# Kernel optimization log

Measured on AMD Instinct MI355X. Metric: run time of the kernel, lower is better.

The kernel has to match this reference:

```python
import jax, jax.numpy as jnp
import numpy as np

Z_INDEX = 0.5  # from init_kwargs


def _masked_mean(v, z_index):
    # Torch: std_mean (unbiased std, ddof=1) over the whole vector, keep values
    # where (v - mean) > -z * std, then mean of kept values. Mask is no_grad.
    mean = jnp.mean(v, axis=-1, keepdims=True)
    std = jnp.std(v, axis=-1, ddof=1, keepdims=True)
    mask = jax.lax.stop_gradient((v - mean) > -z_index * std)  # [B, N] bool
    cnt = jnp.sum(mask, axis=-1).astype(v.dtype)
    return jnp.sum(jnp.where(mask, v, jnp.zeros((), v.dtype)), axis=-1) / cnt


def setup_inputs() -> dict:
    key = jax.random.key(0)
    k1, k2 = jax.random.split(key)
    x = jax.random.normal(k1, (8, 4096, 3), dtype=jnp.float32)
    y = jax.random.normal(k2, (8, 4096, 3), dtype=jnp.float32)
    return {"x": x, "y": y}


def reference(x, y):
    # Pairwise squared Euclidean distances: [B, N, M]
    x2 = jnp.sum(x * x, axis=-1)  # [B, N]
    y2 = jnp.sum(y * y, axis=-1)  # [B, M]
    xy = jnp.einsum('bnd,bmd->bnm', x, y)  # [B, N, M]
    d2 = x2[:, :, None] + y2[:, None, :] - 2.0 * xy
    # directed_distance(S1, S2, mean=False): per-point min squared distance
    dist_to_y = jnp.min(d2, axis=2)  # [B, N] each x-point's nearest y
    dist_to_x = jnp.min(d2, axis=1)  # [B, M] each y-point's nearest x
    # per-batch Z-masked means, summed, then mean over batch
    per_batch = _masked_mean(dist_to_y, Z_INDEX) + _masked_mean(dist_to_x, Z_INDEX)
    return jnp.mean(per_batch)
```

## Files before the change

### kernel.cpp

```cpp
#include <hip/hip_runtime.h>

#define NPTS 4096
#define BATCH 8
#define BLK 256
#define PPT 8
#define NPB (BLK * PPT)
#define MCH 256
#define NCHUNK (NPTS / MCH)
#define PGRP (NPTS / NPB)
#define FBLK 1024

__global__ __launch_bounds__(BLK, 2) void dmin_kernel(
    const float* __restrict__ X, const float* __restrict__ Y,
    float* __restrict__ partial, unsigned int* __restrict__ ticket) {
  if (blockIdx.x == 0 && blockIdx.y == 0 && blockIdx.z == 0 &&
      threadIdx.x == 0) {
    __hip_atomic_store(ticket, 0u, __ATOMIC_RELAXED, __HIP_MEMORY_SCOPE_AGENT);
  }

  const int pg    = blockIdx.x;
  const int b     = blockIdx.y;
  const int chunk = blockIdx.z & (NCHUNK - 1);
  const int dir   = blockIdx.z >> 4;
  const float* pts = dir ? Y : X;
  const float* oth = dir ? X : Y;

  __shared__ float4 s[MCH];
  const float* othb = oth + ((size_t)b * NPTS + (size_t)chunk * MCH) * 3;
  {
    const int i = threadIdx.x;
    float qx = othb[3 * i], qy = othb[3 * i + 1], qz = othb[3 * i + 2];
    s[i] = make_float4(-2.f * qx, -2.f * qy, -2.f * qz,
                       qx * qx + qy * qy + qz * qz);
  }
  __syncthreads();

  const int n0 = pg * NPB + threadIdx.x * PPT;
  const float4* pv4 = (const float4*)(pts + ((size_t)b * NPTS + n0) * 3);
  const float4 A = pv4[0], B = pv4[1], C = pv4[2];
  const float4 D = pv4[3], E = pv4[4], F = pv4[5];
  float px[PPT], py[PPT], pz[PPT];
  px[0] = A.x; py[0] = A.y; pz[0] = A.z;
  px[1] = A.w; py[1] = B.x; pz[1] = B.y;
  px[2] = B.z; py[2] = B.w; pz[2] = C.x;
  px[3] = C.y; py[3] = C.z; pz[3] = C.w;
  px[4] = D.x; py[4] = D.y; pz[4] = D.z;
  px[5] = D.w; py[5] = E.x; pz[5] = E.y;
  px[6] = E.z; py[6] = E.w; pz[6] = F.x;
  px[7] = F.y; py[7] = F.z; pz[7] = F.w;

  float acc[2 * PPT];
#pragma unroll
  for (int i = 0; i < 2 * PPT; ++i) acc[i] = 3.4e38f;

#define COMPUTE(q0, q1, q2, q3)                                               \
  {                                                                           \
    _Pragma("unroll")                                                         \
    for (int pp = 0; pp < PPT; ++pp) {                                        \
      float d0 = fmaf(px[pp], q0.x,                                           \
                 fmaf(py[pp], q0.y, fmaf(pz[pp], q0.z, q0.w)));               \
      float d1 = fmaf(px[pp], q1.x,                                           \
                 fmaf(py[pp], q1.y, fmaf(pz[pp], q1.z, q1.w)));               \
      float d2 = fmaf(px[pp], q2.x,                                           \
                 fmaf(py[pp], q2.y, fmaf(pz[pp], q2.z, q2.w)));               \
      float d3 = fmaf(px[pp], q3.x,                                           \
                 fmaf(py[pp], q3.y, fmaf(pz[pp], q3.z, q3.w)));               \
      acc[2 * pp]     = fminf(fminf(acc[2 * pp], d0), d1);        \
      acc[2 * pp + 1] = fminf(fminf(acc[2 * pp + 1], d2), d3);    \
    }                                                                         \
  }

  float4 c0 = s[0], c1 = s[1], c2 = s[2], c3 = s[3];
#pragma unroll 2
  for (int m = 0; m < MCH - 4; m += 4) {
    float4 t0 = s[m + 4], t1 = s[m + 5], t2 = s[m + 6], t3 = s[m + 7];
    COMPUTE(c0, c1, c2, c3);
    c0 = t0; c1 = t1; c2 = t2; c3 = t3;
  }
  COMPUTE(c0, c1, c2, c3);
#undef COMPUTE

  float r[PPT];
#pragma unroll
  for (int pp = 0; pp < PPT; ++pp) {
    float c = px[pp] * px[pp] + py[pp] * py[pp] + pz[pp] * pz[pp];
    r[pp] = fminf(acc[2 * pp], acc[2 * pp + 1]) + c;
  }
  float* dst = &partial[(((size_t)chunk * 2 + dir) * BATCH + b) * NPTS + n0];
  ((float4*)dst)[0] = make_float4(r[0], r[1], r[2], r[3]);
  ((float4*)dst)[1] = make_float4(r[4], r[5], r[6], r[7]);
}

__global__ __launch_bounds__(FBLK) void finalize_kernel(
    const float* __restrict__ partial, float* __restrict__ res,
    unsigned int* __restrict__ ticket, float* __restrict__ out) {
  const int w    = blockIdx.x;
  const int dir  = w >> 3;
  const int b    = w & 7;
  const int wid  = threadIdx.x >> 6;
  const int lane = threadIdx.x & 63;

  __shared__ float rA[16], rB[16], rC[16], rD[16];

  const float4* pv = (const float4*)partial;
  const size_t vbase = ((size_t)dir * BATCH + b) * (NPTS / 4);
  const size_t cstr  = (size_t)2 * BATCH * (NPTS / 4);

  float4 m = pv[vbase + threadIdx.x];
#pragma unroll
  for (int c = 1; c < NCHUNK; ++c) {
    float4 t = pv[vbase + (size_t)c * cstr + threadIdx.x];
    m.x = fminf(m.x, t.x); m.y = fminf(m.y, t.y);
    m.z = fminf(m.z, t.z); m.w = fminf(m.w, t.w);
  }
  float sum = (m.x + m.y) + (m.z + m.w);
  float ssq = (m.x * m.x + m.y * m.y) + (m.z * m.z + m.w * m.w);

  for (int off = 32; off; off >>= 1) sum += __shfl_xor(sum, off, 64);
  for (int off = 32; off; off >>= 1) ssq += __shfl_xor(ssq, off, 64);
  if (lane == 0) { rA[wid] = sum; rB[wid] = ssq; }
  __syncthreads();
  sum = ((rA[0] + rA[1]) + (rA[2] + rA[3])) + ((rA[4] + rA[5]) + (rA[6] + rA[7]))
      + ((rA[8] + rA[9]) + (rA[10] + rA[11])) + ((rA[12] + rA[13]) + (rA[14] + rA[15]));
  ssq = ((rB[0] + rB[1]) + (rB[2] + rB[3])) + ((rB[4] + rB[5]) + (rB[6] + rB[7]))
      + ((rB[8] + rB[9]) + (rB[10] + rB[11])) + ((rB[12] + rB[13]) + (rB[14] + rB[15]));
  const float mean = sum / (float)NPTS;
  const float var  = (ssq - (float)NPTS * mean * mean) / (float)(NPTS - 1);
  const float neg_thr = -0.5f * sqrtf(fmaxf(var, 0.0f));

  float ksum = 0.0f, kcnt = 0.0f;
  if (m.x - mean > neg_thr) { ksum += m.x; kcnt += 1.0f; }
  if (m.y - mean > neg_thr) { ksum += m.y; kcnt += 1.0f; }
  if (m.z - mean > neg_thr) { ksum += m.z; kcnt += 1.0f; }
  if (m.w - mean > neg_thr) { ksum += m.w; kcnt += 1.0f; }
  for (int off = 32; off; off >>= 1) ksum += __shfl_xor(ksum, off, 64);
  for (int off = 32; off; off >>= 1) kcnt += __shfl_xor(kcnt, off, 64);
  if (lane == 0) { rC[wid] = ksum; rD[wid] = kcnt; }
  __syncthreads();

  if (threadIdx.x == 0) {
    ksum = ((rC[0] + rC[1]) + (rC[2] + rC[3])) + ((rC[4] + rC[5]) + (rC[6] + rC[7]))
         + ((rC[8] + rC[9]) + (rC[10] + rC[11])) + ((rC[12] + rC[13]) + (rC[14] + rC[15]));
    kcnt = ((rD[0] + rD[1]) + (rD[2] + rD[3])) + ((rD[4] + rD[5]) + (rD[6] + rD[7]))
         + ((rD[8] + rD[9]) + (rD[10] + rD[11])) + ((rD[12] + rD[13]) + (rD[14] + rD[15]));
    __hip_atomic_store(&res[w], ksum / kcnt, __ATOMIC_RELAXED,
                       __HIP_MEMORY_SCOPE_AGENT);
    __threadfence();
    unsigned int old = atomicAdd(ticket, 1u);
    if (old == 15u) {
      __threadfence();
      float tot = 0.0f;
      for (int i = 0; i < 16; ++i) {
        tot += __hip_atomic_load(&res[i], __ATOMIC_RELAXED,
                                 __HIP_MEMORY_SCOPE_AGENT);
      }
      out[0] = tot / (float)BATCH;
    }
  }
}

extern "C" void kernel_launch(void* const* d_in, const int* in_sizes, int n_in,
                              void* d_out, int out_size, void* d_ws, size_t ws_size,
                              hipStream_t stream) {
  const float* x = (const float*)d_in[0];
  const float* y = (const float*)d_in[1];
  float* out = (float*)d_out;
  float* partial = (float*)d_ws;
  float* res = partial + (size_t)NCHUNK * 2 * BATCH * NPTS;
  unsigned int* ticket = (unsigned int*)(res + 16);

  dim3 g1(PGRP, BATCH, 2 * NCHUNK);
  dmin_kernel<<<g1, BLK, 0, stream>>>(x, y, partial, ticket);
  finalize_kernel<<<16, FBLK, 0, stream>>>(partial, res, ticket, out);
}
```

Baseline: 32.78 us.

## Cover both directions and all points in one 1024-thread block per chunk

The distance kernel now launches one 1024-thread block per (batch, chunk). Half the threads handle the x→y direction and half handle y→x, each thread covering 8 points of the full 4096-point set. The chunk size drops from 256 to 128, so the grid has 256 blocks instead of 512, and both directions' query tiles are staged in shared memory together. This halves the number of blocks and staging loads, but doubles the partial buffer the finalize kernel must reduce (32 chunks). It also uses larger blocks, which may change occupancy.

```diff
diff --git a/kernel.cpp b/kernel.cpp
--- a/kernel.cpp
+++ b/kernel.cpp
@@ -2,40 +2,40 @@
 
 #define NPTS 4096
 #define BATCH 8
-#define BLK 256
+#define BLK 1024
 #define PPT 8
-#define NPB (BLK * PPT)
-#define MCH 256
+#define MCH 128
 #define NCHUNK (NPTS / MCH)
-#define PGRP (NPTS / NPB)
 #define FBLK 1024
 
-__global__ __launch_bounds__(BLK, 2) void dmin_kernel(
+__global__ __launch_bounds__(BLK, 4) void dmin_kernel(
     const float* __restrict__ X, const float* __restrict__ Y,
     float* __restrict__ partial, unsigned int* __restrict__ ticket) {
-  if (blockIdx.x == 0 && blockIdx.y == 0 && blockIdx.z == 0 &&
-      threadIdx.x == 0) {
+  if (blockIdx.x == 0 && blockIdx.y == 0 && threadIdx.x == 0) {
     __hip_atomic_store(ticket, 0u, __ATOMIC_RELAXED, __HIP_MEMORY_SCOPE_AGENT);
   }
 
-  const int pg    = blockIdx.x;
-  const int b     = blockIdx.y;
-  const int chunk = blockIdx.z & (NCHUNK - 1);
-  const int dir   = blockIdx.z >> 4;
-  const float* pts = dir ? Y : X;
-  const float* oth = dir ? X : Y;
+  const int b     = blockIdx.x;
+  const int chunk = blockIdx.y;
+  const int dir   = threadIdx.x >> 9;
+  const int t     = threadIdx.x & 511;
 
-  __shared__ float4 s[MCH];
-  const float* othb = oth + ((size_t)b * NPTS + (size_t)chunk * MCH) * 3;
-  {
-    const int i = threadIdx.x;
-    float qx = othb[3 * i], qy = othb[3 * i + 1], qz = othb[3 * i + 2];
-    s[i] = make_float4(-2.f * qx, -2.f * qy, -2.f * qz,
-                       qx * qx + qy * qy + qz * qz);
+  __shared__ float4 s[2 * MCH];
+  if (threadIdx.x < 2 * MCH) {
+    const int which = threadIdx.x >> 7;
+    const int i     = threadIdx.x & (MCH - 1);
+    const float* src = which ? X : Y;
+    const float* qb  = src + ((size_t)b * NPTS + (size_t)chunk * MCH) * 3;
+    float qx = qb[3 * i], qy = qb[3 * i + 1], qz = qb[3 * i + 2];
+    s[threadIdx.x] = make_float4(-2.f * qx, -2.f * qy, -2.f * qz,
+                                 qx * qx + qy * qy + qz * qz);
   }
   __syncthreads();
 
-  const int n0 = pg * NPB + threadIdx.x * PPT;
+  const float* pts = dir ? Y : X;
+  const float4* sq = &s[dir ? MCH : 0];
+
+  const int n0 = t * PPT;
   const float4* pv4 = (const float4*)(pts + ((size_t)b * NPTS + n0) * 3);
   const float4 A = pv4[0], B = pv4[1], C = pv4[2];
   const float4 D = pv4[3], E = pv4[4], F = pv4[5];
@@ -70,10 +70,10 @@
     }                                                                         \
   }
 
-  float4 c0 = s[0], c1 = s[1], c2 = s[2], c3 = s[3];
+  float4 c0 = sq[0], c1 = sq[1], c2 = sq[2], c3 = sq[3];
 #pragma unroll 2
   for (int m = 0; m < MCH - 4; m += 4) {
-    float4 t0 = s[m + 4], t1 = s[m + 5], t2 = s[m + 6], t3 = s[m + 7];
+    float4 t0 = sq[m + 4], t1 = sq[m + 5], t2 = sq[m + 6], t3 = sq[m + 7];
     COMPUTE(c0, c1, c2, c3);
     c0 = t0; c1 = t1; c2 = t2; c3 = t3;
   }
@@ -169,7 +169,7 @@
   float* res = partial + (size_t)NCHUNK * 2 * BATCH * NPTS;
   unsigned int* ticket = (unsigned int*)(res + 16);
 
-  dim3 g1(PGRP, BATCH, 2 * NCHUNK);
+  dim3 g1(BATCH, NCHUNK);
   dmin_kernel<<<g1, BLK, 0, stream>>>(x, y, partial, ticket);
   finalize_kernel<<<16, FBLK, 0, stream>>>(partial, res, ticket, out);
 }
```

After: 33.90 us. +3.4%, slower.
